# Optimization experiments

Hardware: AMD Instinct MI355X
Metric: run time of the kernel (lower is better)

The kernel has to match this reference:

```python
import jax, jax.numpy as jnp
import numpy as np

NUM_HEADS = 16
HEAD_DIM = 64  # hidden_size 1024 / 16 heads


def setup_inputs() -> dict:
    key = jax.random.key(0)
    ks = jax.random.split(key, 9)
    B, T, H = 8, 4096, 1024
    s = 1.0 / np.sqrt(H)
    return {
        "hidden_states": jax.random.normal(ks[0], (B, T + 1, H), jnp.float32),
        "cell_state": jax.random.normal(ks[1], (B, H), jnp.float32),
        "Wq": jax.random.normal(ks[2], (H, H), jnp.float32) * s,
        "bq": jax.random.normal(ks[3], (H,), jnp.float32) * 0.02,
        "Wk": jax.random.normal(ks[4], (H, H), jnp.float32) * s,
        "bk": jax.random.normal(ks[5], (H,), jnp.float32) * 0.02,
        "Wv": jax.random.normal(ks[6], (H, H), jnp.float32) * s,
        "bv": jax.random.normal(ks[7], (H,), jnp.float32) * 0.02,
        "attention_mask": jax.random.randint(ks[8], (B, T), 0, 2, jnp.int32),
        "t": T,
    }


def reference(hidden_states, cell_state, Wq, bq, Wk, bk, Wv, bv, attention_mask, t):
    B, _, H = hidden_states.shape
    nh, hd = NUM_HEADS, HEAD_DIM
    # single-query projection: [B, H] -> [B, nh, hd]
    q = (cell_state @ Wq.T + bq).reshape(B, nh, hd)
    # key/value over first t positions: [B, t, H] -> [B, t, nh, hd]
    kv_in = hidden_states[:, :-1]
    k = (kv_in @ Wk.T + bk).reshape(B, t, nh, hd)
    v = (kv_in @ Wv.T + bv).reshape(B, t, nh, hd)
    # GEMV-like scores: [B, nh, t]
    scores = jnp.einsum("bhd,bthd->bht", q, k) / np.sqrt(hd)
    # mask out positions where attention_mask == 0 (intended semantics of
    # inf * eq(mask, 0) in the original, expressed without -inf*0 NaNs)
    mask_add = jnp.where(attention_mask == 0, -jnp.inf, 0.0)[:, None, :]
    probs = jax.nn.softmax(scores + mask_add, axis=-1)
    # dropout is identity in eval mode
    ctx = jnp.einsum("bht,bthd->bhd", probs, v)  # [B, nh, hd]
    return ctx.reshape(B, nh * hd)  # squeeze of [B, 1, H]
```

## Files before the change

kernel.cpp:

```cpp
#include <hip/hip_runtime.h>
#include <math.h>

#define BB 8
#define TT 4096
#define TP1 4097
#define HH 1024
#define NHD 16

__device__ __forceinline__ float dot4(const float4& a, const float4& b) {
  return a.x*b.x + a.y*b.y + a.z*b.z + a.w*b.w;
}

__global__ __launch_bounds__(256) void k_q(const float* __restrict__ cell,
                                           const float* __restrict__ Wq,
                                           const float* __restrict__ bq,
                                           float* __restrict__ qbuf) {
  __shared__ float cs[BB * HH];
  int tid = threadIdx.x;
  #pragma unroll
  for (int m = 0; m < 8; m++) {
    int idx4 = tid + 256 * m;
    ((float4*)cs)[idx4] = ((const float4*)cell)[idx4];
  }
  __syncthreads();
  int jj = tid >> 4, qq = tid & 15;
  int j = blockIdx.x * 16 + jj;
  float acc[BB];
  #pragma unroll
  for (int b = 0; b < BB; b++) acc[b] = 0.f;
  #pragma unroll
  for (int k = 0; k < 16; k++) {
    int i = qq * 4 + 64 * k;
    float4 w = *(const float4*)&Wq[(size_t)j * HH + i];
    #pragma unroll
    for (int b = 0; b < BB; b++) {
      float4 c = *(const float4*)&cs[b * HH + i];
      acc[b] += dot4(w, c);
    }
  }
  #pragma unroll
  for (int b = 0; b < BB; b++) {
    acc[b] += __shfl_xor(acc[b], 1);
    acc[b] += __shfl_xor(acc[b], 2);
    acc[b] += __shfl_xor(acc[b], 4);
    acc[b] += __shfl_xor(acc[b], 8);
  }
  if (qq == 0) {
    float bqv = bq[j];
    #pragma unroll
    for (int b = 0; b < BB; b++) qbuf[b * HH + j] = 0.125f * (acc[b] + bqv);
  }
}

__global__ __launch_bounds__(256) void k_qwk(const float* __restrict__ qbuf,
                                             const float* __restrict__ Wk,
                                             const float* __restrict__ bk,
                                             float* __restrict__ qWkT,
                                             float* __restrict__ qbk) {
  __shared__ float q_s[BB * 64];
  __shared__ float bk_s[64];
  int tid = threadIdx.x;
  int h = blockIdx.x >> 2, ic = blockIdx.x & 3;
  if (tid < 128) {
    int b = tid >> 4, d4 = tid & 15;
    *(float4*)&q_s[b * 64 + d4 * 4] = *(const float4*)&qbuf[b * HH + h * 64 + d4 * 4];
  }
  if (tid >= 128 && tid < 144) {
    int d4 = tid - 128;
    *(float4*)&bk_s[d4 * 4] = *(const float4*)&bk[h * 64 + d4 * 4];
  }
  __syncthreads();
  int i = ic * 256 + tid;
  float acc[BB];
  #pragma unroll
  for (int b = 0; b < BB; b++) acc[b] = 0.f;
  for (int d = 0; d < 64; d++) {
    float wk = Wk[(size_t)(h * 64 + d) * HH + i];
    #pragma unroll
    for (int b = 0; b < BB; b++) acc[b] += q_s[b * 64 + d] * wk;
  }
  #pragma unroll
  for (int b = 0; b < BB; b++) qWkT[((size_t)b * HH + i) * NHD + h] = acc[b];
  if (ic == 0 && tid < 8) {
    float s = 0.f;
    for (int d = 0; d < 64; d++) s += q_s[tid * 64 + d] * bk_s[d];
    qbk[tid * NHD + h] = s;
  }
}

__global__ __launch_bounds__(256) void k_scores(const float* __restrict__ hid,
                                                const float* __restrict__ qWkT,
                                                const float* __restrict__ qbk,
                                                const int* __restrict__ mask,
                                                float* __restrict__ probsT,
                                                float* __restrict__ Spart) {
  __shared__ float red[4 * 64 * NHD];
  __shared__ float e_s[64 * NHD];
  __shared__ float qbk_s[NHD];
  int tid = threadIdx.x;
  int b = blockIdx.x >> 6, tile = blockIdx.x & 63;
  if (tid < NHD) qbk_s[tid] = qbk[b * NHD + tid];
  int w = __builtin_amdgcn_readfirstlane(tid >> 6);
  int lane = tid & 63;
  int t = tile * 64 + lane;
  const float4* rowp = (const float4*)(hid + (size_t)(b * TP1 + t) * HH + (w << 8));
  const float* qwt = qWkT + (size_t)((b << 10) + (w << 8)) * NHD;
  float acc[NHD];
  #pragma unroll
  for (int h = 0; h < NHD; h++) acc[h] = 0.f;
  #pragma unroll 2
  for (int ic = 0; ic < 64; ic++) {
    float4 kv = rowp[ic];
    const float* qp = qwt + (ic << 6);
    #pragma unroll
    for (int h = 0; h < NHD; h++)
      acc[h] += kv.x * qp[h] + kv.y * qp[NHD + h] +
                kv.z * qp[2 * NHD + h] + kv.w * qp[3 * NHD + h];
  }
  #pragma unroll
  for (int h4 = 0; h4 < 4; h4++)
    *(float4*)&red[((w << 6) + lane) * NHD + (h4 << 2)] =
        make_float4(acc[h4 * 4], acc[h4 * 4 + 1], acc[h4 * 4 + 2], acc[h4 * 4 + 3]);
  __syncthreads();
  int row = tid >> 2, hq = tid & 3;
  float4 s = make_float4(0.f, 0.f, 0.f, 0.f);
  #pragma unroll
  for (int ww = 0; ww < 4; ww++) {
    float4 r = *(const float4*)&red[((ww << 6) + row) * NHD + (hq << 2)];
    s.x += r.x; s.y += r.y; s.z += r.z; s.w += r.w;
  }
  int mk = mask[b * TT + tile * 64 + row];
  float4 e;
  e.x = mk ? __expf(s.x + qbk_s[hq * 4 + 0]) : 0.f;
  e.y = mk ? __expf(s.y + qbk_s[hq * 4 + 1]) : 0.f;
  e.z = mk ? __expf(s.z + qbk_s[hq * 4 + 2]) : 0.f;
  e.w = mk ? __expf(s.w + qbk_s[hq * 4 + 3]) : 0.f;
  *(float4*)&probsT[(size_t)(b * TT + tile * 64 + row) * NHD + (hq << 2)] = e;
  *(float4*)&e_s[row * NHD + (hq << 2)] = e;
  __syncthreads();
  if (tid < 64) {
    int g = tid >> 4, h2 = tid & 15;
    float s2 = 0.f;
    #pragma unroll
    for (int j = 0; j < 16; j++) s2 += e_s[((g + (j << 2)) << 4) + h2];
    s2 += __shfl_xor(s2, 16);
    s2 += __shfl_xor(s2, 32);
    if (tid < 16) Spart[(size_t)((b << 6) + tile) * NHD + h2] = s2;
  }
}

__global__ void k_sinv(const float* __restrict__ Spart, float* __restrict__ Sinv) {
  int tid = threadIdx.x;
  float s = 0.f;
  for (int c = 0; c < 64; c++) s += Spart[(size_t)((tid >> 4) * 64 + c) * NHD + (tid & 15)];
  Sinv[tid] = 1.f / s;
}

__global__ __launch_bounds__(256) void k_ctx(const float* __restrict__ hid,
                                             const float* __restrict__ probsT,
                                             float* __restrict__ ctxpart) {
  __shared__ float red[4 * 64 * NHD];
  int tid = threadIdx.x;
  int b = blockIdx.x >> 5, ic = (blockIdx.x >> 1) & 15, th = blockIdx.x & 1;
  int w = __builtin_amdgcn_readfirstlane(tid >> 6);
  int lane = tid & 63;
  int i = (ic << 6) + lane;
  const float* kvp = hid + (size_t)b * TP1 * HH + i;
  const float* pb = probsT + (size_t)b * TT * NHD;
  int t0 = (th << 11) + w;
  float acc[NHD];
  #pragma unroll
  for (int h = 0; h < NHD; h++) acc[h] = 0.f;
  #pragma unroll 4
  for (int it = 0; it < 512; it++) {
    int t = t0 + (it << 2);
    float kv = kvp[(size_t)t * HH];
    const float* pp = pb + t * NHD;
    #pragma unroll
    for (int h = 0; h < NHD; h++) acc[h] += kv * pp[h];
  }
  #pragma unroll
  for (int h4 = 0; h4 < 4; h4++)
    *(float4*)&red[((w << 6) + lane) * NHD + (h4 << 2)] =
        make_float4(acc[h4 * 4], acc[h4 * 4 + 1], acc[h4 * 4 + 2], acc[h4 * 4 + 3]);
  __syncthreads();
  int ii = tid >> 2, hq = tid & 3;
  float4 s = make_float4(0.f, 0.f, 0.f, 0.f);
  #pragma unroll
  for (int ww = 0; ww < 4; ww++) {
    float4 r = *(const float4*)&red[((ww << 6) + ii) * NHD + (hq << 2)];
    s.x += r.x; s.y += r.y; s.z += r.z; s.w += r.w;
  }
  size_t base = ((size_t)(th * BB + b) * NHD + (hq << 2)) * HH + (ic << 6) + ii;
  ctxpart[base] = s.x;
  ctxpart[base + HH] = s.y;
  ctxpart[base + 2 * HH] = s.z;
  ctxpart[base + 3 * HH] = s.w;
}

__global__ __launch_bounds__(256) void k_out(const float* __restrict__ Wv,
                                             const float* __restrict__ bv,
                                             const float* __restrict__ ctxpart,
                                             const float* __restrict__ Sinv,
                                             float* __restrict__ out) {
  __shared__ float cs[BB * HH];
  int tid = threadIdx.x;
  int j0 = blockIdx.x * 16;
  int h = j0 >> 6;
  const float4* cp4 = (const float4*)ctxpart;
  #pragma unroll
  for (int m = 0; m < 8; m++) {
    int idx4 = tid + 256 * m;
    int b = idx4 >> 8, i4 = idx4 & 255;
    float4 p0 = cp4[(((size_t)(0 * BB + b) * NHD + h) << 8) + i4];
    float4 p1 = cp4[(((size_t)(1 * BB + b) * NHD + h) << 8) + i4];
    ((float4*)cs)[idx4] = make_float4(p0.x + p1.x, p0.y + p1.y, p0.z + p1.z, p0.w + p1.w);
  }
  __syncthreads();
  int jj = tid >> 4, qq = tid & 15;
  int j = j0 + jj;
  float acc[BB];
  #pragma unroll
  for (int b = 0; b < BB; b++) acc[b] = 0.f;
  #pragma unroll
  for (int k = 0; k < 16; k++) {
    int i = qq * 4 + 64 * k;
    float4 w = *(const float4*)&Wv[(size_t)j * HH + i];
    #pragma unroll
    for (int b = 0; b < BB; b++) {
      float4 c = *(const float4*)&cs[b * HH + i];
      acc[b] += dot4(w, c);
    }
  }
  #pragma unroll
  for (int b = 0; b < BB; b++) {
    acc[b] += __shfl_xor(acc[b], 1);
    acc[b] += __shfl_xor(acc[b], 2);
    acc[b] += __shfl_xor(acc[b], 4);
    acc[b] += __shfl_xor(acc[b], 8);
  }
  if (qq == 0) {
    float bvj = bv[j];
    #pragma unroll
    for (int b = 0; b < BB; b++)
      out[b * HH + j] = Sinv[b * NHD + h] * acc[b] + bvj;
  }
}

extern "C" void kernel_launch(void* const* d_in, const int* in_sizes, int n_in,
                              void* d_out, int out_size, void* d_ws, size_t ws_size,
                              hipStream_t stream) {
  const float* hid  = (const float*)d_in[0];
  const float* cell = (const float*)d_in[1];
  const float* Wq   = (const float*)d_in[2];
  const float* bq   = (const float*)d_in[3];
  const float* Wk   = (const float*)d_in[4];
  const float* bk   = (const float*)d_in[5];
  const float* Wv   = (const float*)d_in[6];
  const float* bv   = (const float*)d_in[7];
  const int*  mask  = (const int*)d_in[8];
  float* out = (float*)d_out;

  float* ws = (float*)d_ws;
  float* qbuf    = ws;
  float* qWkT    = ws + 8192;
  float* qbk     = ws + 139264;
  float* probsT  = ws + 139392;
  float* Spart   = ws + 663680;
  float* Sinv    = ws + 671872;
  float* ctxpart = ws + 672000;

  hipLaunchKernelGGL(k_q,      dim3(64),  dim3(256), 0, stream, cell, Wq, bq, qbuf);
  hipLaunchKernelGGL(k_qwk,    dim3(64),  dim3(256), 0, stream, qbuf, Wk, bk, qWkT, qbk);
  hipLaunchKernelGGL(k_scores, dim3(512), dim3(256), 0, stream, hid, qWkT, qbk, mask, probsT, Spart);
  hipLaunchKernelGGL(k_sinv,   dim3(1),   dim3(128), 0, stream, Spart, Sinv);
  hipLaunchKernelGGL(k_ctx,    dim3(256), dim3(256), 0, stream, hid, probsT, ctxpart);
  hipLaunchKernelGGL(k_out,    dim3(64),  dim3(256), 0, stream, Wv, bv, ctxpart, Sinv, out);
}
```

Before: 304.3 us.

## Stage score tiles through LDS, vectorize ctx pass with atomics, widen small GEMV grids

The scores kernel now loads each 64-row tile of hidden states into padded, double-buffered shared memory before computing. Each thread then reads from LDS instead of doing strided per-thread global row loads. The ctx kernel switches to float4 loads along the hidden dimension over 512 blocks and accumulates partial sums into a zeroed buffer with atomicAdd, replacing the two-way partial buffer. The q, qWk and output GEMV kernels use 4x more blocks, with one wavefront per output row and a full-wave shuffle reduction. The risks are float atomic contention and order nondeterminism, the extra memset, and added barriers in the scores loop.

```diff
diff --git a/kernel.cpp b/kernel.cpp
--- a/kernel.cpp
+++ b/kernel.cpp
@@ -19,33 +19,29 @@
   int tid = threadIdx.x;
   #pragma unroll
   for (int m = 0; m < 8; m++) {
-    int idx4 = tid + 256 * m;
+    int idx4 = tid + (m << 8);
     ((float4*)cs)[idx4] = ((const float4*)cell)[idx4];
   }
   __syncthreads();
-  int jj = tid >> 4, qq = tid & 15;
-  int j = blockIdx.x * 16 + jj;
+  int jj = tid >> 6, lane = tid & 63;
+  int j = blockIdx.x * 4 + jj;
   float acc[BB];
   #pragma unroll
   for (int b = 0; b < BB; b++) acc[b] = 0.f;
   #pragma unroll
-  for (int k = 0; k < 16; k++) {
-    int i = qq * 4 + 64 * k;
+  for (int k = 0; k < 4; k++) {
+    int i = (k << 8) + (lane << 2);
     float4 w = *(const float4*)&Wq[(size_t)j * HH + i];
     #pragma unroll
-    for (int b = 0; b < BB; b++) {
-      float4 c = *(const float4*)&cs[b * HH + i];
-      acc[b] += dot4(w, c);
-    }
+    for (int b = 0; b < BB; b++) acc[b] += dot4(w, *(const float4*)&cs[b * HH + i]);
   }
   #pragma unroll
   for (int b = 0; b < BB; b++) {
-    acc[b] += __shfl_xor(acc[b], 1);
-    acc[b] += __shfl_xor(acc[b], 2);
-    acc[b] += __shfl_xor(acc[b], 4);
-    acc[b] += __shfl_xor(acc[b], 8);
-  }
-  if (qq == 0) {
+    acc[b] += __shfl_xor(acc[b], 1);  acc[b] += __shfl_xor(acc[b], 2);
+    acc[b] += __shfl_xor(acc[b], 4);  acc[b] += __shfl_xor(acc[b], 8);
+    acc[b] += __shfl_xor(acc[b], 16); acc[b] += __shfl_xor(acc[b], 32);
+  }
+  if (lane == 0) {
     float bqv = bq[j];
     #pragma unroll
     for (int b = 0; b < BB; b++) qbuf[b * HH + j] = 0.125f * (acc[b] + bqv);
@@ -58,33 +54,67 @@
                                              float* __restrict__ qWkT,
                                              float* __restrict__ qbk) {
   __shared__ float q_s[BB * 64];
-  __shared__ float bk_s[64];
-  int tid = threadIdx.x;
-  int h = blockIdx.x >> 2, ic = blockIdx.x & 3;
+  __shared__ float red[4 * 64 * 9];
+  int tid = threadIdx.x;
+  int h = blockIdx.x >> 4, ic = blockIdx.x & 15;
   if (tid < 128) {
-    int b = tid >> 4, d4 = tid & 15;
-    *(float4*)&q_s[b * 64 + d4 * 4] = *(const float4*)&qbuf[b * HH + h * 64 + d4 * 4];
-  }
-  if (tid >= 128 && tid < 144) {
-    int d4 = tid - 128;
-    *(float4*)&bk_s[d4 * 4] = *(const float4*)&bk[h * 64 + d4 * 4];
-  }
-  __syncthreads();
-  int i = ic * 256 + tid;
+    int b = tid >> 4, dq = tid & 15;
+    ((float4*)q_s)[tid] = ((const float4*)qbuf)[(b << 8) + (h << 4) + dq];
+  }
+  __syncthreads();
+  int dg = tid >> 6, lane = tid & 63;
+  int i = (ic << 6) + lane;
   float acc[BB];
   #pragma unroll
   for (int b = 0; b < BB; b++) acc[b] = 0.f;
-  for (int d = 0; d < 64; d++) {
-    float wk = Wk[(size_t)(h * 64 + d) * HH + i];
-    #pragma unroll
-    for (int b = 0; b < BB; b++) acc[b] += q_s[b * 64 + d] * wk;
-  }
-  #pragma unroll
-  for (int b = 0; b < BB; b++) qWkT[((size_t)b * HH + i) * NHD + h] = acc[b];
+  #pragma unroll
+  for (int dd = 0; dd < 16; dd++) {
+    int d = (dg << 4) + dd;
+    float wk = Wk[(size_t)((h << 6) + d) * HH + i];
+    #pragma unroll
+    for (int b = 0; b < BB; b++) acc[b] += q_s[(b << 6) + d] * wk;
+  }
+  #pragma unroll
+  for (int b = 0; b < BB; b++) red[((dg << 6) + lane) * 9 + b] = acc[b];
+  __syncthreads();
+  #pragma unroll
+  for (int r = 0; r < 2; r++) {
+    int o = tid + (r << 8);
+    int il = o >> 3, b = o & 7;
+    float s = 0.f;
+    #pragma unroll
+    for (int g = 0; g < 4; g++) s += red[((g << 6) + il) * 9 + b];
+    qWkT[((size_t)(b << 10) + (ic << 6) + il) * NHD + h] = s;
+  }
   if (ic == 0 && tid < 8) {
     float s = 0.f;
-    for (int d = 0; d < 64; d++) s += q_s[tid * 64 + d] * bk_s[d];
+    for (int d = 0; d < 64; d++) s += q_s[(tid << 6) + d] * bk[(h << 6) + d];
     qbk[tid * NHD + h] = s;
+  }
+}
+
+__device__ __forceinline__ void stage_tile(const float* __restrict__ src, float* dst, int tid) {
+  #pragma unroll
+  for (int m = 0; m < 4; m++) {
+    int idx = tid + (m << 8);
+    int r = idx >> 4, c4 = idx & 15;
+    *(float4*)&dst[r * 68 + (c4 << 2)] = *(const float4*)&src[(size_t)r * HH + (c4 << 2)];
+  }
+}
+
+__device__ __forceinline__ void compute_chunk(const float* kv_s, const float* __restrict__ qb,
+                                              int lane, int w, float* acc) {
+  float4 kv[4];
+  #pragma unroll
+  for (int cq = 0; cq < 4; cq++)
+    kv[cq] = *(const float4*)&kv_s[lane * 68 + (w << 4) + (cq << 2)];
+  #pragma unroll
+  for (int cq = 0; cq < 4; cq++) {
+    const float* qp = qb + (cq << 6);
+    #pragma unroll
+    for (int h = 0; h < NHD; h++)
+      acc[h] += kv[cq].x * qp[h] + kv[cq].y * qp[NHD + h] +
+                kv[cq].z * qp[2 * NHD + h] + kv[cq].w * qp[3 * NHD + h];
   }
 }
 
@@ -94,29 +124,34 @@
                                                 const int* __restrict__ mask,
                                                 float* __restrict__ probsT,
                                                 float* __restrict__ Spart) {
-  __shared__ float red[4 * 64 * NHD];
-  __shared__ float e_s[64 * NHD];
+  __shared__ float kv0[64 * 68];
+  __shared__ float kv1[64 * 68];
   __shared__ float qbk_s[NHD];
   int tid = threadIdx.x;
   int b = blockIdx.x >> 6, tile = blockIdx.x & 63;
+  int t0 = tile << 6;
   if (tid < NHD) qbk_s[tid] = qbk[b * NHD + tid];
   int w = __builtin_amdgcn_readfirstlane(tid >> 6);
   int lane = tid & 63;
-  int t = tile * 64 + lane;
-  const float4* rowp = (const float4*)(hid + (size_t)(b * TP1 + t) * HH + (w << 8));
-  const float* qwt = qWkT + (size_t)((b << 10) + (w << 8)) * NHD;
+  const float* src = hid + ((size_t)(b * TP1) + t0) * HH;
+  const float* qB = qWkT + (((size_t)(b << 10) + (w << 4)) << 4);
   float acc[NHD];
   #pragma unroll
   for (int h = 0; h < NHD; h++) acc[h] = 0.f;
-  #pragma unroll 2
-  for (int ic = 0; ic < 64; ic++) {
-    float4 kv = rowp[ic];
-    const float* qp = qwt + (ic << 6);
-    #pragma unroll
-    for (int h = 0; h < NHD; h++)
-      acc[h] += kv.x * qp[h] + kv.y * qp[NHD + h] +
-                kv.z * qp[2 * NHD + h] + kv.w * qp[3 * NHD + h];
-  }
+
+  stage_tile(src, kv0, tid);
+  __syncthreads();
+  for (int cc = 0; cc < 16; cc += 2) {
+    stage_tile(src + ((cc + 1) << 6), kv1, tid);
+    compute_chunk(kv0, qB + ((cc << 6) << 4), lane, w, acc);
+    __syncthreads();
+    if (cc + 2 < 16) stage_tile(src + ((cc + 2) << 6), kv0, tid);
+    compute_chunk(kv1, qB + (((cc + 1) << 6) << 4), lane, w, acc);
+    __syncthreads();
+  }
+
+  float* red = kv0;
+  float* e_sh = kv1;
   #pragma unroll
   for (int h4 = 0; h4 < 4; h4++)
     *(float4*)&red[((w << 6) + lane) * NHD + (h4 << 2)] =
@@ -129,20 +164,20 @@
     float4 r = *(const float4*)&red[((ww << 6) + row) * NHD + (hq << 2)];
     s.x += r.x; s.y += r.y; s.z += r.z; s.w += r.w;
   }
-  int mk = mask[b * TT + tile * 64 + row];
+  int mk = mask[b * TT + t0 + row];
   float4 e;
   e.x = mk ? __expf(s.x + qbk_s[hq * 4 + 0]) : 0.f;
   e.y = mk ? __expf(s.y + qbk_s[hq * 4 + 1]) : 0.f;
   e.z = mk ? __expf(s.z + qbk_s[hq * 4 + 2]) : 0.f;
   e.w = mk ? __expf(s.w + qbk_s[hq * 4 + 3]) : 0.f;
-  *(float4*)&probsT[(size_t)(b * TT + tile * 64 + row) * NHD + (hq << 2)] = e;
-  *(float4*)&e_s[row * NHD + (hq << 2)] = e;
+  *(float4*)&probsT[((size_t)(b * TT + t0 + row)) * NHD + (hq << 2)] = e;
+  *(float4*)&e_sh[row * NHD + (hq << 2)] = e;
   __syncthreads();
   if (tid < 64) {
     int g = tid >> 4, h2 = tid & 15;
     float s2 = 0.f;
     #pragma unroll
-    for (int j = 0; j < 16; j++) s2 += e_s[((g + (j << 2)) << 4) + h2];
+    for (int j = 0; j < 16; j++) s2 += e_sh[((g + (j << 2)) << 4) + h2];
     s2 += __shfl_xor(s2, 16);
     s2 += __shfl_xor(s2, 32);
     if (tid < 16) Spart[(size_t)((b << 6) + tile) * NHD + h2] = s2;
@@ -158,88 +193,94 @@
 
 __global__ __launch_bounds__(256) void k_ctx(const float* __restrict__ hid,
                                              const float* __restrict__ probsT,
-                                             float* __restrict__ ctxpart) {
-  __shared__ float red[4 * 64 * NHD];
-  int tid = threadIdx.x;
-  int b = blockIdx.x >> 5, ic = (blockIdx.x >> 1) & 15, th = blockIdx.x & 1;
+                                             float* __restrict__ ctxin) {
+  __shared__ float red2[2][64 * 64];
+  int tid = threadIdx.x;
+  int b = blockIdx.x >> 6, ic = (blockIdx.x >> 4) & 3, th = blockIdx.x & 15;
   int w = __builtin_amdgcn_readfirstlane(tid >> 6);
   int lane = tid & 63;
-  int i = (ic << 6) + lane;
-  const float* kvp = hid + (size_t)b * TP1 * HH + i;
-  const float* pb = probsT + (size_t)b * TT * NHD;
-  int t0 = (th << 11) + w;
-  float acc[NHD];
-  #pragma unroll
-  for (int h = 0; h < NHD; h++) acc[h] = 0.f;
+  int t0 = (th << 2) + w;
+  const float* kvp = hid + (size_t)b * TP1 * HH + (ic << 8) + (lane << 2);
+  const float* pb = probsT + ((size_t)(b << 12) + t0) * NHD;
+  float4 acc4[NHD];
+  #pragma unroll
+  for (int h = 0; h < NHD; h++) acc4[h] = make_float4(0.f, 0.f, 0.f, 0.f);
   #pragma unroll 4
-  for (int it = 0; it < 512; it++) {
-    int t = t0 + (it << 2);
-    float kv = kvp[(size_t)t * HH];
-    const float* pp = pb + t * NHD;
-    #pragma unroll
-    for (int h = 0; h < NHD; h++) acc[h] += kv * pp[h];
-  }
-  #pragma unroll
-  for (int h4 = 0; h4 < 4; h4++)
-    *(float4*)&red[((w << 6) + lane) * NHD + (h4 << 2)] =
-        make_float4(acc[h4 * 4], acc[h4 * 4 + 1], acc[h4 * 4 + 2], acc[h4 * 4 + 3]);
-  __syncthreads();
-  int ii = tid >> 2, hq = tid & 3;
-  float4 s = make_float4(0.f, 0.f, 0.f, 0.f);
-  #pragma unroll
-  for (int ww = 0; ww < 4; ww++) {
-    float4 r = *(const float4*)&red[((ww << 6) + ii) * NHD + (hq << 2)];
-    s.x += r.x; s.y += r.y; s.z += r.z; s.w += r.w;
-  }
-  size_t base = ((size_t)(th * BB + b) * NHD + (hq << 2)) * HH + (ic << 6) + ii;
-  ctxpart[base] = s.x;
-  ctxpart[base + HH] = s.y;
-  ctxpart[base + 2 * HH] = s.z;
-  ctxpart[base + 3 * HH] = s.w;
+  for (int it = 0; it < 64; it++) {
+    int t = it << 6;
+    float4 kv = *(const float4*)&kvp[(size_t)(t0 + t) * HH];
+    const float* pp = pb + (size_t)t * NHD;
+    #pragma unroll
+    for (int h = 0; h < NHD; h++) {
+      float p = pp[h];
+      acc4[h].x += kv.x * p; acc4[h].y += kv.y * p;
+      acc4[h].z += kv.z * p; acc4[h].w += kv.w * p;
+    }
+  }
+  if (w < 2) {
+    #pragma unroll
+    for (int h = 0; h < NHD; h++)
+      *(float4*)&red2[w][(lane << 6) + (h << 2)] = acc4[h];
+  }
+  __syncthreads();
+  if (w >= 2) {
+    #pragma unroll
+    for (int h = 0; h < NHD; h++) {
+      float4 r = *(const float4*)&red2[w - 2][(lane << 6) + (h << 2)];
+      r.x += acc4[h].x; r.y += acc4[h].y; r.z += acc4[h].z; r.w += acc4[h].w;
+      *(float4*)&red2[w - 2][(lane << 6) + (h << 2)] = r;
+    }
+  }
+  __syncthreads();
+  #pragma unroll
+  for (int j = 0; j < 4; j++) {
+    int k = tid + (j << 8);
+    float4 a = ((const float4*)red2[0])[k];
+    float4 c2 = ((const float4*)red2[1])[k];
+    int li = k >> 4, h = k & 15;
+    float* dst = ctxin + (((size_t)(b << 4) + h) << 10) + (ic << 8) + (li << 2);
+    atomicAdd(dst + 0, a.x + c2.x);
+    atomicAdd(dst + 1, a.y + c2.y);
+    atomicAdd(dst + 2, a.z + c2.z);
+    atomicAdd(dst + 3, a.w + c2.w);
+  }
 }
 
 __global__ __launch_bounds__(256) void k_out(const float* __restrict__ Wv,
                                              const float* __restrict__ bv,
-                                             const float* __restrict__ ctxpart,
+                                             const float* __restrict__ ctxin,
                                              const float* __restrict__ Sinv,
                                              float* __restrict__ out) {
   __shared__ float cs[BB * HH];
   int tid = threadIdx.x;
-  int j0 = blockIdx.x * 16;
-  int h = j0 >> 6;
-  const float4* cp4 = (const float4*)ctxpart;
+  int h = blockIdx.x >> 4;
+  int j0 = blockIdx.x * 4;
   #pragma unroll
   for (int m = 0; m < 8; m++) {
-    int idx4 = tid + 256 * m;
+    int idx4 = tid + (m << 8);
     int b = idx4 >> 8, i4 = idx4 & 255;
-    float4 p0 = cp4[(((size_t)(0 * BB + b) * NHD + h) << 8) + i4];
-    float4 p1 = cp4[(((size_t)(1 * BB + b) * NHD + h) << 8) + i4];
-    ((float4*)cs)[idx4] = make_float4(p0.x + p1.x, p0.y + p1.y, p0.z + p1.z, p0.w + p1.w);
-  }
-  __syncthreads();
-  int jj = tid >> 4, qq = tid & 15;
+    ((float4*)cs)[idx4] = ((const float4*)ctxin)[(((b << 4) + h) << 8) + i4];
+  }
+  __syncthreads();
+  int jj = tid >> 6, lane = tid & 63;
   int j = j0 + jj;
   float acc[BB];
   #pragma unroll
   for (int b = 0; b < BB; b++) acc[b] = 0.f;
   #pragma unroll
-  for (int k = 0; k < 16; k++) {
-    int i = qq * 4 + 64 * k;
+  for (int k = 0; k < 4; k++) {
+    int i = (k << 8) + (lane << 2);
     float4 w = *(const float4*)&Wv[(size_t)j * HH + i];
     #pragma unroll
-    for (int b = 0; b < BB; b++) {
-      float4 c = *(const float4*)&cs[b * HH + i];
-      acc[b] += dot4(w, c);
-    }
+    for (int b = 0; b < BB; b++) acc[b] += dot4(w, *(const float4*)&cs[b * HH + i]);
   }
   #pragma unroll
   for (int b = 0; b < BB; b++) {
-    acc[b] += __shfl_xor(acc[b], 1);
-    acc[b] += __shfl_xor(acc[b], 2);
-    acc[b] += __shfl_xor(acc[b], 4);
-    acc[b] += __shfl_xor(acc[b], 8);
-  }
-  if (qq == 0) {
+    acc[b] += __shfl_xor(acc[b], 1);  acc[b] += __shfl_xor(acc[b], 2);
+    acc[b] += __shfl_xor(acc[b], 4);  acc[b] += __shfl_xor(acc[b], 8);
+    acc[b] += __shfl_xor(acc[b], 16); acc[b] += __shfl_xor(acc[b], 32);
+  }
+  if (lane == 0) {
     float bvj = bv[j];
     #pragma unroll
     for (int b = 0; b < BB; b++)
@@ -268,12 +309,13 @@
   float* probsT  = ws + 139392;
   float* Spart   = ws + 663680;
   float* Sinv    = ws + 671872;
-  float* ctxpart = ws + 672000;
-
-  hipLaunchKernelGGL(k_q,      dim3(64),  dim3(256), 0, stream, cell, Wq, bq, qbuf);
-  hipLaunchKernelGGL(k_qwk,    dim3(64),  dim3(256), 0, stream, qbuf, Wk, bk, qWkT, qbk);
+  float* ctxin   = ws + 672000;
+
+  hipMemsetAsync(ctxin, 0, (size_t)BB * NHD * HH * sizeof(float), stream);
+  hipLaunchKernelGGL(k_q,      dim3(256), dim3(256), 0, stream, cell, Wq, bq, qbuf);
+  hipLaunchKernelGGL(k_qwk,    dim3(256), dim3(256), 0, stream, qbuf, Wk, bk, qWkT, qbk);
   hipLaunchKernelGGL(k_scores, dim3(512), dim3(256), 0, stream, hid, qWkT, qbk, mask, probsT, Spart);
   hipLaunchKernelGGL(k_sinv,   dim3(1),   dim3(128), 0, stream, Spart, Sinv);
-  hipLaunchKernelGGL(k_ctx,    dim3(256), dim3(256), 0, stream, hid, probsT, ctxpart);
-  hipLaunchKernelGGL(k_out,    dim3(64),  dim3(256), 0, stream, Wv, bv, ctxpart, Sinv, out);
-}
+  hipLaunchKernelGGL(k_ctx,    dim3(512), dim3(256), 0, stream, hid, probsT, ctxin);
+  hipLaunchKernelGGL(k_out,    dim3(256), dim3(256), 0, stream, Wv, bv, ctxin, Sinv, out);
+}
```

Measured after the change: 295.4 us. 1.03x faster.
